# Kernel tuning notes

Measured on AMD Instinct MI355X. Metric: run time of the kernel, lower is better.

The kernel has to match this reference:

```python
import jax, jax.numpy as jnp
import numpy as np

DIM = 1024
NUM_HEADS = 16
HEAD_DIM = DIM // NUM_HEADS


def setup_inputs() -> dict:
    key = jax.random.key(0)
    k1, k2, k3, k4, k5 = jax.random.split(key, 5)
    scale = 0.02
    return {
        "x": jax.random.normal(k1, (4, 2048, DIM), dtype=jnp.float32),
        "w_qkv": jax.random.normal(k2, (DIM, 3 * DIM), dtype=jnp.float32) * scale,
        "b_qkv": jax.random.normal(k3, (3 * DIM,), dtype=jnp.float32) * scale,
        "w_proj": jax.random.normal(k4, (DIM, DIM), dtype=jnp.float32) * scale,
        "b_proj": jax.random.normal(k5, (DIM,), dtype=jnp.float32) * scale,
    }


def reference(x, w_qkv, b_qkv, w_proj, b_proj):
    B, N, C = x.shape
    H, D = NUM_HEADS, HEAD_DIM
    qkv = x @ w_qkv + b_qkv                      # [B, N, 3C]
    qkv = qkv.reshape(B, N, 3, H, D)
    q = qkv[:, :, 0].transpose(0, 2, 1, 3)       # [B, H, N, D]
    k = qkv[:, :, 1].transpose(0, 2, 1, 3)
    v = qkv[:, :, 2].transpose(0, 2, 1, 3)
    attn = jnp.einsum("bhnd,bhmd->bhnm", q, k) / (D ** 0.5)  # [B, H, N, N]
    attn = jax.nn.softmax(attn, axis=-1)
    out = jnp.einsum("bhnm,bhmd->bhnd", attn, v)  # [B, H, N, D]
    out = out.transpose(0, 2, 1, 3).reshape(B, N, C)
    return out @ w_proj + b_proj
```

## Files before the change

### kernel.cpp

```cpp
#include <hip/hip_runtime.h>
#include <stdint.h>

typedef __bf16 bf16_t;
typedef __bf16 bf16x8 __attribute__((ext_vector_type(8)));
typedef __bf16 bf16x4 __attribute__((ext_vector_type(4)));
typedef float  f32x4  __attribute__((ext_vector_type(4)));

__device__ __forceinline__ void g2l16(const void* g, void* l) {
    __builtin_amdgcn_global_load_lds(
        (const __attribute__((address_space(1))) unsigned int*)g,
        (__attribute__((address_space(3))) unsigned int*)l, 16, 0, 0);
}

__global__ __launch_bounds__(256) void prep_kernel(
    const float* __restrict__ x, const float* __restrict__ w_qkv,
    const float* __restrict__ w_proj,
    bf16_t* __restrict__ x_bf, bf16_t* __restrict__ wqkvT, bf16_t* __restrict__ wprojT)
{
    __shared__ float t[32][33];
    const int bx = blockIdx.x;
    if (bx < 8192) {
        const int idx = (bx * 256 + threadIdx.x) * 4;
        const float4 v = *(const float4*)(x + idx);
        bf16x4 o;
        o[0] = (bf16_t)v.x; o[1] = (bf16_t)v.y; o[2] = (bf16_t)v.z; o[3] = (bf16_t)v.w;
        *(bf16x4*)(x_bf + idx) = o;
        return;
    }
    const float* in;
    bf16_t* outp;
    int c0, r0, C;
    if (bx < 11264) {
        const int b = bx - 8192;
        in = w_qkv; outp = wqkvT; C = 3072;
        c0 = (b % 96) * 32; r0 = (b / 96) * 32;
    } else {
        const int b = bx - 11264;
        in = w_proj; outp = wprojT; C = 1024;
        c0 = (b & 31) * 32; r0 = (b >> 5) * 32;
    }
    const int xx = threadIdx.x & 31, y = threadIdx.x >> 5;
    #pragma unroll
    for (int i = 0; i < 32; i += 8)
        t[y + i][xx] = in[(size_t)(r0 + y + i) * C + c0 + xx];
    __syncthreads();
    #pragma unroll
    for (int i = 0; i < 32; i += 8)
        outp[(size_t)(c0 + y + i) * 1024 + r0 + xx] = (bf16_t)t[xx][y + i];
}

__device__ __forceinline__ void gemm128(
    const bf16_t* __restrict__ A, const bf16_t* __restrict__ Bt, const int K,
    bf16_t* sA, bf16_t* sB, const int m0, const int n0, f32x4 acc[4][4])
{
    const int tid  = threadIdx.x;
    const int lane = tid & 63;
    const int w    = tid >> 6;
    const int wm   = (w >> 1) * 64;
    const int wn   = (w & 1) * 64;
    const int col0 = lane & 15;
    const int quad = lane >> 4;

    #pragma unroll
    for (int mt = 0; mt < 4; ++mt)
        #pragma unroll
        for (int nt = 0; nt < 4; ++nt)
            acc[mt][nt] = (f32x4){0.f, 0.f, 0.f, 0.f};

    const int srow = tid >> 3;
    const int jsw  = ((tid & 7) ^ (srow & 7)) << 3;
    const bf16_t* Ab = A  + (size_t)(m0 + srow) * K + jsw;
    const bf16_t* Bb = Bt + (size_t)(n0 + srow) * K + jsw;

    for (int kb = 0; kb < K; kb += 64) {
        #pragma unroll
        for (int it = 0; it < 4; ++it) {
            g2l16(Ab + (size_t)(it * 32) * K + kb, sA + (size_t)(it * 256 + tid) * 8);
            g2l16(Bb + (size_t)(it * 32) * K + kb, sB + (size_t)(it * 256 + tid) * 8);
        }
        __syncthreads();
        #pragma unroll
        for (int ks = 0; ks < 2; ++ks) {
            const int jg = ks * 4 + quad;
            bf16x8 af[4], bv[4];
            #pragma unroll
            for (int mt = 0; mt < 4; ++mt) {
                const int ra = wm + mt * 16 + col0;
                af[mt] = *(const bf16x8*)(sA + ra * 64 + ((jg ^ (ra & 7)) << 3));
            }
            #pragma unroll
            for (int nt = 0; nt < 4; ++nt) {
                const int rb = wn + nt * 16 + col0;
                bv[nt] = *(const bf16x8*)(sB + rb * 64 + ((jg ^ (rb & 7)) << 3));
            }
            #pragma unroll
            for (int mt = 0; mt < 4; ++mt)
                #pragma unroll
                for (int nt = 0; nt < 4; ++nt)
                    acc[mt][nt] = __builtin_amdgcn_mfma_f32_16x16x32_bf16(
                        af[mt], bv[nt], acc[mt][nt], 0, 0, 0);
        }
        __syncthreads();
    }
}

#define QSCALE 0.18033688f
__global__ __launch_bounds__(256) void qkv_gemm_kernel(
    const bf16_t* __restrict__ x, const bf16_t* __restrict__ wT,
    const float* __restrict__ bias,
    bf16_t* __restrict__ q, bf16_t* __restrict__ k, bf16_t* __restrict__ vT)
{
    __shared__ bf16_t sA[128 * 64];
    __shared__ bf16_t sB[128 * 64];
    const int m0 = blockIdx.y * 128;
    const int n0 = blockIdx.x * 128;
    f32x4 acc[4][4];
    gemm128(x, wT, 1024, sA, sB, m0, n0, acc);

    const int tid = threadIdx.x, lane = tid & 63, w = tid >> 6;
    const int wm = (w >> 1) * 64, wn = (w & 1) * 64;
    const int col0 = lane & 15, quad = lane >> 4;
    const int sel = n0 >> 10;

    #pragma unroll
    for (int mt = 0; mt < 4; ++mt) {
        const int m_base = m0 + wm + mt * 16 + quad * 4;
        const int b = m_base >> 11;
        const int t = m_base & 2047;
        #pragma unroll
        for (int nt = 0; nt < 4; ++nt) {
            const int n = n0 + wn + nt * 16 + col0;
            const float bvv = bias[n];
            const int h = (n >> 6) & 15, d = n & 63;
            const size_t bh = (size_t)b * 16 + h;
            if (sel == 0) {
                #pragma unroll
                for (int r = 0; r < 4; ++r)
                    q[(bh * 2048 + t + r) * 64 + d] = (bf16_t)((acc[mt][nt][r] + bvv) * QSCALE);
            } else if (sel == 1) {
                #pragma unroll
                for (int r = 0; r < 4; ++r)
                    k[(bh * 2048 + t + r) * 64 + d] = (bf16_t)(acc[mt][nt][r] + bvv);
            } else {
                #pragma unroll
                for (int r = 0; r < 4; ++r)
                    vT[(bh * 64 + d) * 2048 + t + r] = (bf16_t)(acc[mt][nt][r] + bvv);
            }
        }
    }
}

__global__ __launch_bounds__(256) void proj_gemm_kernel(
    const bf16_t* __restrict__ a, const bf16_t* __restrict__ wT,
    const float* __restrict__ bias, float* __restrict__ out)
{
    __shared__ bf16_t sA[128 * 64];
    __shared__ bf16_t sB[128 * 64];
    const int m0 = blockIdx.y * 128;
    const int n0 = blockIdx.x * 128;
    f32x4 acc[4][4];
    gemm128(a, wT, 1024, sA, sB, m0, n0, acc);

    const int tid = threadIdx.x, lane = tid & 63, w = tid >> 6;
    const int wm = (w >> 1) * 64, wn = (w & 1) * 64;
    const int col0 = lane & 15, quad = lane >> 4;
    #pragma unroll
    for (int mt = 0; mt < 4; ++mt) {
        const int m_base = m0 + wm + mt * 16 + quad * 4;
        #pragma unroll
        for (int nt = 0; nt < 4; ++nt) {
            const int n = n0 + wn + nt * 16 + col0;
            const float bvv = bias[n];
            #pragma unroll
            for (int r = 0; r < 4; ++r)
                out[(size_t)(m_base + r) * 1024 + n] = acc[mt][nt][r] + bvv;
        }
    }
}

#define SP_STRIDE 72
__global__ __launch_bounds__(256, 3) void attn_kernel(
    const bf16_t* __restrict__ q, const bf16_t* __restrict__ k,
    const bf16_t* __restrict__ vT, bf16_t* __restrict__ out)
{
    __shared__ __align__(16) char smem[18432 + 16384 + 16384];
    bf16_t* sQ = (bf16_t*)smem;
    bf16_t* sP = (bf16_t*)smem;
    bf16_t* sK = (bf16_t*)(smem + 18432);
    bf16_t* sV = (bf16_t*)(smem + 18432 + 16384);

    const int x   = blockIdx.x;
    const int loc = x >> 3;
    const int qb  = loc & 15;
    const int bh  = (x & 7) + ((loc >> 4) << 3);

    const int tid = threadIdx.x, lane = tid & 63, w = tid >> 6;
    const int col0 = lane & 15, quad = lane >> 4;

    const bf16_t* qbase = q  + ((size_t)bh * 2048 + qb * 128) * 64;
    const bf16_t* kbase = k  + (size_t)bh * 2048 * 64;
    const bf16_t* vbase = vT + (size_t)bh * 64 * 2048;

    const int srow8  = tid >> 3;
    const int jsw8   = ((tid & 7) ^ (srow8 & 7)) << 3;
    const int srow16 = tid >> 4;
    const int jsw16  = ((tid & 15) ^ (srow16 & 15)) << 3;

    #pragma unroll
    for (int it = 0; it < 4; ++it)
        g2l16(qbase + (size_t)(it * 32 + srow8) * 64 + jsw8,
              sQ + (size_t)(it * 256 + tid) * 8);

    bf16x8 kr[4], vr[4];
    #pragma unroll
    for (int it = 0; it < 4; ++it)
        kr[it] = *(const bf16x8*)(kbase + (size_t)(it * 32 + srow8) * 64 + jsw8);
    #pragma unroll
    for (int it = 0; it < 4; ++it)
        vr[it] = *(const bf16x8*)(vbase + (size_t)(it * 16 + srow16) * 2048 + jsw16);

    __syncthreads();

    bf16x8 qf[2][2];
    #pragma unroll
    for (int mt = 0; mt < 2; ++mt)
        #pragma unroll
        for (int ks = 0; ks < 2; ++ks) {
            const int rq = w * 32 + mt * 16 + col0;
            const int jg = ks * 4 + quad;
            qf[mt][ks] = *(const bf16x8*)(sQ + rq * 64 + ((jg ^ (rq & 7)) << 3));
        }

    f32x4 oacc[2][4];
    float row_l[2][4];
    #pragma unroll
    for (int mt = 0; mt < 2; ++mt) {
        #pragma unroll
        for (int nt = 0; nt < 4; ++nt) oacc[mt][nt] = (f32x4){0.f, 0.f, 0.f, 0.f};
        #pragma unroll
        for (int r = 0; r < 4; ++r) row_l[mt][r] = 0.f;
    }

    for (int kv = 0; kv < 16; ++kv) {
        __syncthreads();
        #pragma unroll
        for (int it = 0; it < 4; ++it)
            *(bf16x8*)(sK + (size_t)(it * 256 + tid) * 8) = kr[it];
        #pragma unroll
        for (int it = 0; it < 4; ++it)
            *(bf16x8*)(sV + (size_t)(it * 256 + tid) * 8) = vr[it];
        __syncthreads();

        const int kvn = (kv < 15) ? kv + 1 : 15;
        const bf16_t* kg = kbase + (size_t)kvn * 128 * 64;
        #pragma unroll
        for (int it = 0; it < 4; ++it)
            kr[it] = *(const bf16x8*)(kg + (size_t)(it * 32 + srow8) * 64 + jsw8);
        #pragma unroll
        for (int it = 0; it < 4; ++it)
            vr[it] = *(const bf16x8*)(vbase + (size_t)(it * 16 + srow16) * 2048
                                      + kvn * 128 + jsw16);

        f32x4 s[2][8];
        #pragma unroll
        for (int mt = 0; mt < 2; ++mt)
            #pragma unroll
            for (int nt = 0; nt < 8; ++nt) s[mt][nt] = (f32x4){0.f, 0.f, 0.f, 0.f};
        #pragma unroll
        for (int ks = 0; ks < 2; ++ks) {
            const int jg = ks * 4 + quad;
            bf16x8 kf[8];
            #pragma unroll
            for (int nt = 0; nt < 8; ++nt) {
                const int rk = nt * 16 + col0;
                kf[nt] = *(const bf16x8*)(sK + rk * 64 + ((jg ^ (rk & 7)) << 3));
            }
            #pragma unroll
            for (int mt = 0; mt < 2; ++mt)
                #pragma unroll
                for (int nt = 0; nt < 8; ++nt)
                    s[mt][nt] = __builtin_amdgcn_mfma_f32_16x16x32_bf16(
                        qf[mt][ks], kf[nt], s[mt][nt], 0, 0, 0);
        }

        #pragma unroll
        for (int mt = 0; mt < 2; ++mt)
            #pragma unroll
            for (int r = 0; r < 4; ++r) {
                float rs = 0.f;
                #pragma unroll
                for (int nt = 0; nt < 8; ++nt) {
                    const float p = __builtin_amdgcn_exp2f(s[mt][nt][r]);
                    s[mt][nt][r] = p;
                    rs += p;
                }
                row_l[mt][r] += rs;
            }

        #pragma unroll
        for (int half = 0; half < 2; ++half) {
            #pragma unroll
            for (int mt = 0; mt < 2; ++mt)
                #pragma unroll
                for (int nt = 0; nt < 4; ++nt)
                    #pragma unroll
                    for (int r = 0; r < 4; ++r)
                        sP[(w * 32 + mt * 16 + quad * 4 + r) * SP_STRIDE + nt * 16 + col0] =
                            (bf16_t)s[mt][half * 4 + nt][r];
            #pragma unroll
            for (int ks = 0; ks < 2; ++ks) {
                bf16x8 pf[2], vf[4];
                #pragma unroll
                for (int mt = 0; mt < 2; ++mt)
                    pf[mt] = *(const bf16x8*)(sP + (w * 32 + mt * 16 + col0) * SP_STRIDE
                                              + ks * 32 + quad * 8);
                #pragma unroll
                for (int nt = 0; nt < 4; ++nt) {
                    const int dv = nt * 16 + col0;
                    const int jg = half * 8 + ks * 4 + quad;
                    vf[nt] = *(const bf16x8*)(sV + dv * 128 + ((jg ^ (dv & 15)) << 3));
                }
                #pragma unroll
                for (int mt = 0; mt < 2; ++mt)
                    #pragma unroll
                    for (int nt = 0; nt < 4; ++nt)
                        oacc[mt][nt] = __builtin_amdgcn_mfma_f32_16x16x32_bf16(
                            pf[mt], vf[nt], oacc[mt][nt], 0, 0, 0);
            }
        }
    }

    const int b = bh >> 4, h = bh & 15;
    #pragma unroll
    for (int mt = 0; mt < 2; ++mt) {
        #pragma unroll
        for (int r = 0; r < 4; ++r) {
            float l = row_l[mt][r];
            #pragma unroll
            for (int off = 1; off < 16; off <<= 1) l += __shfl_xor(l, off);
            const float inv = 1.0f / l;
            const int t = qb * 128 + w * 32 + mt * 16 + quad * 4 + r;
            const size_t rowbase = ((size_t)b * 2048 + t) * 1024 + h * 64;
            #pragma unroll
            for (int nt = 0; nt < 4; ++nt)
                out[rowbase + nt * 16 + col0] = (bf16_t)(oacc[mt][nt][r] * inv);
        }
    }
}

extern "C" void kernel_launch(void* const* d_in, const int* in_sizes, int n_in,
                              void* d_out, int out_size, void* d_ws, size_t ws_size,
                              hipStream_t stream) {
    const float* x      = (const float*)d_in[0];
    const float* w_qkv  = (const float*)d_in[1];
    const float* b_qkv  = (const float*)d_in[2];
    const float* w_proj = (const float*)d_in[3];
    const float* b_proj = (const float*)d_in[4];
    float* out = (float*)d_out;

    char* p = (char*)d_ws;
    bf16_t* x_bf   = (bf16_t*)p; p += (size_t)8192 * 1024 * 2;
    bf16_t* wqkvT  = (bf16_t*)p; p += (size_t)3072 * 1024 * 2;
    bf16_t* wprojT = (bf16_t*)p; p += (size_t)1024 * 1024 * 2;
    bf16_t* qb     = (bf16_t*)p; p += (size_t)8192 * 1024 * 2;
    bf16_t* kb     = (bf16_t*)p; p += (size_t)8192 * 1024 * 2;
    bf16_t* vTb    = (bf16_t*)p; p += (size_t)8192 * 1024 * 2;
    bf16_t* attb   = (bf16_t*)p; p += (size_t)8192 * 1024 * 2;

    prep_kernel<<<12288, 256, 0, stream>>>(x, w_qkv, w_proj, x_bf, wqkvT, wprojT);
    qkv_gemm_kernel<<<dim3(24, 64), 256, 0, stream>>>(x_bf, wqkvT, b_qkv, qb, kb, vTb);
    attn_kernel<<<1024, 256, 0, stream>>>(qb, kb, vTb, attb);
    proj_gemm_kernel<<<dim3(8, 64), 256, 0, stream>>>(attb, wprojT, b_proj, out);
}
```

Measured before the change: 279.7 us.

## Keep softmax probabilities in registers via transposed QK^T and permlane swaps

Computes S transposed (K as the A operand, Q as B) so that each lane holds the scores for a single query row, then converts the probabilities to packed bf16 and rearranges them across lanes with permlane32/16 swaps into the A-operand layout of the PV MFMA. This removes the shared-memory P buffer and its store/load round trip; Q is now loaded straight from global into registers, dropping the Q LDS staging and one barrier. LDS use per block shrinks, which may allow more resident blocks. The lane-shuffle mapping is subtle, and the row-sum reduction now goes through a different shuffle pattern.

```diff
diff --git a/kernel.cpp b/kernel.cpp
--- a/kernel.cpp
+++ b/kernel.cpp
@@ -178,16 +178,13 @@
     }
 }
 
-#define SP_STRIDE 72
 __global__ __launch_bounds__(256, 3) void attn_kernel(
     const bf16_t* __restrict__ q, const bf16_t* __restrict__ k,
     const bf16_t* __restrict__ vT, bf16_t* __restrict__ out)
 {
-    __shared__ __align__(16) char smem[18432 + 16384 + 16384];
-    bf16_t* sQ = (bf16_t*)smem;
-    bf16_t* sP = (bf16_t*)smem;
-    bf16_t* sK = (bf16_t*)(smem + 18432);
-    bf16_t* sV = (bf16_t*)(smem + 18432 + 16384);
+    __shared__ __align__(16) char smem[16384 + 16384];
+    bf16_t* sK = (bf16_t*)smem;
+    bf16_t* sV = (bf16_t*)(smem + 16384);
 
     const int x   = blockIdx.x;
     const int loc = x >> 3;
@@ -206,10 +203,13 @@
     const int srow16 = tid >> 4;
     const int jsw16  = ((tid & 15) ^ (srow16 & 15)) << 3;
 
-    #pragma unroll
-    for (int it = 0; it < 4; ++it)
-        g2l16(qbase + (size_t)(it * 32 + srow8) * 64 + jsw8,
-              sQ + (size_t)(it * 256 + tid) * 8);
+    bf16x8 qf[2][2];
+    #pragma unroll
+    for (int mt = 0; mt < 2; ++mt)
+        #pragma unroll
+        for (int ks = 0; ks < 2; ++ks)
+            qf[mt][ks] = *(const bf16x8*)(qbase
+                + (size_t)(w * 32 + mt * 16 + col0) * 64 + ks * 32 + quad * 8);
 
     bf16x8 kr[4], vr[4];
     #pragma unroll
@@ -219,26 +219,13 @@
     for (int it = 0; it < 4; ++it)
         vr[it] = *(const bf16x8*)(vbase + (size_t)(it * 16 + srow16) * 2048 + jsw16);
 
-    __syncthreads();
-
-    bf16x8 qf[2][2];
-    #pragma unroll
-    for (int mt = 0; mt < 2; ++mt)
-        #pragma unroll
-        for (int ks = 0; ks < 2; ++ks) {
-            const int rq = w * 32 + mt * 16 + col0;
-            const int jg = ks * 4 + quad;
-            qf[mt][ks] = *(const bf16x8*)(sQ + rq * 64 + ((jg ^ (rq & 7)) << 3));
-        }
-
     f32x4 oacc[2][4];
-    float row_l[2][4];
+    float row_l[2];
     #pragma unroll
     for (int mt = 0; mt < 2; ++mt) {
         #pragma unroll
         for (int nt = 0; nt < 4; ++nt) oacc[mt][nt] = (f32x4){0.f, 0.f, 0.f, 0.f};
-        #pragma unroll
-        for (int r = 0; r < 4; ++r) row_l[mt][r] = 0.f;
+        row_l[mt] = 0.f;
     }
 
     for (int kv = 0; kv < 16; ++kv) {
@@ -261,84 +248,95 @@
             vr[it] = *(const bf16x8*)(vbase + (size_t)(it * 16 + srow16) * 2048
                                       + kvn * 128 + jsw16);
 
-        f32x4 s[2][8];
-        #pragma unroll
-        for (int mt = 0; mt < 2; ++mt)
-            #pragma unroll
-            for (int nt = 0; nt < 8; ++nt) s[mt][nt] = (f32x4){0.f, 0.f, 0.f, 0.f};
-        #pragma unroll
-        for (int ks = 0; ks < 2; ++ks) {
-            const int jg = ks * 4 + quad;
-            bf16x8 kf[8];
-            #pragma unroll
-            for (int nt = 0; nt < 8; ++nt) {
-                const int rk = nt * 16 + col0;
-                kf[nt] = *(const bf16x8*)(sK + rk * 64 + ((jg ^ (rk & 7)) << 3));
-            }
-            #pragma unroll
-            for (int mt = 0; mt < 2; ++mt)
-                #pragma unroll
-                for (int nt = 0; nt < 8; ++nt)
-                    s[mt][nt] = __builtin_amdgcn_mfma_f32_16x16x32_bf16(
-                        qf[mt][ks], kf[nt], s[mt][nt], 0, 0, 0);
-        }
-
-        #pragma unroll
-        for (int mt = 0; mt < 2; ++mt)
-            #pragma unroll
-            for (int r = 0; r < 4; ++r) {
-                float rs = 0.f;
-                #pragma unroll
-                for (int nt = 0; nt < 8; ++nt) {
-                    const float p = __builtin_amdgcn_exp2f(s[mt][nt][r]);
-                    s[mt][nt][r] = p;
-                    rs += p;
+        #pragma unroll
+        for (int hf = 0; hf < 2; ++hf) {
+            f32x4 s[4][2];
+            #pragma unroll
+            for (int nt = 0; nt < 4; ++nt)
+                #pragma unroll
+                for (int mt = 0; mt < 2; ++mt) s[nt][mt] = (f32x4){0.f, 0.f, 0.f, 0.f};
+            #pragma unroll
+            for (int ks = 0; ks < 2; ++ks) {
+                const int jg = ks * 4 + quad;
+                bf16x8 kf[4];
+                #pragma unroll
+                for (int nt = 0; nt < 4; ++nt) {
+                    const int rk = hf * 64 + nt * 16 + col0;
+                    kf[nt] = *(const bf16x8*)(sK + rk * 64 + ((jg ^ (rk & 7)) << 3));
                 }
-                row_l[mt][r] += rs;
-            }
-
-        #pragma unroll
-        for (int half = 0; half < 2; ++half) {
-            #pragma unroll
-            for (int mt = 0; mt < 2; ++mt)
                 #pragma unroll
                 for (int nt = 0; nt < 4; ++nt)
                     #pragma unroll
-                    for (int r = 0; r < 4; ++r)
-                        sP[(w * 32 + mt * 16 + quad * 4 + r) * SP_STRIDE + nt * 16 + col0] =
-                            (bf16_t)s[mt][half * 4 + nt][r];
-            #pragma unroll
-            for (int ks = 0; ks < 2; ++ks) {
-                bf16x8 pf[2], vf[4];
-                #pragma unroll
-                for (int mt = 0; mt < 2; ++mt)
-                    pf[mt] = *(const bf16x8*)(sP + (w * 32 + mt * 16 + col0) * SP_STRIDE
-                                              + ks * 32 + quad * 8);
+                    for (int mt = 0; mt < 2; ++mt)
+                        s[nt][mt] = __builtin_amdgcn_mfma_f32_16x16x32_bf16(
+                            kf[nt], qf[mt][ks], s[nt][mt], 0, 0, 0);
+            }
+
+            unsigned pw[2][2][4];
+            #pragma unroll
+            for (int mt = 0; mt < 2; ++mt) {
+                #pragma unroll
+                for (int kp = 0; kp < 2; ++kp) {
+                    float p0[4], p1[4];
+                    float rs = 0.f;
+                    #pragma unroll
+                    for (int r = 0; r < 4; ++r) {
+                        p0[r] = __builtin_amdgcn_exp2f(s[2 * kp][mt][r]);
+                        p1[r] = __builtin_amdgcn_exp2f(s[2 * kp + 1][mt][r]);
+                        rs += p0[r] + p1[r];
+                    }
+                    row_l[mt] += rs;
+                    unsigned XA, XB, YA, YB;
+                    asm("v_cvt_pk_bf16_f32 %0, %1, %2" : "=v"(XA) : "v"(p0[0]), "v"(p0[1]));
+                    asm("v_cvt_pk_bf16_f32 %0, %1, %2" : "=v"(XB) : "v"(p0[2]), "v"(p0[3]));
+                    asm("v_cvt_pk_bf16_f32 %0, %1, %2" : "=v"(YA) : "v"(p1[0]), "v"(p1[1]));
+                    asm("v_cvt_pk_bf16_f32 %0, %1, %2" : "=v"(YB) : "v"(p1[2]), "v"(p1[3]));
+                    asm("v_permlane32_swap_b32 %0, %1" : "+v"(XA), "+v"(YA));
+                    asm("v_permlane16_swap_b32 %0, %1" : "+v"(XA), "+v"(YA));
+                    asm("v_permlane32_swap_b32 %0, %1" : "+v"(XB), "+v"(YB));
+                    asm("v_permlane16_swap_b32 %0, %1" : "+v"(XB), "+v"(YB));
+                    pw[mt][kp][0] = XA; pw[mt][kp][1] = XB;
+                    pw[mt][kp][2] = YA; pw[mt][kp][3] = YB;
+                }
+            }
+
+            #pragma unroll
+            for (int kp = 0; kp < 2; ++kp) {
+                const int jg2 = (hf * 2 + kp) * 4 + quad;
+                bf16x8 vf[4];
                 #pragma unroll
                 for (int nt = 0; nt < 4; ++nt) {
                     const int dv = nt * 16 + col0;
-                    const int jg = half * 8 + ks * 4 + quad;
-                    vf[nt] = *(const bf16x8*)(sV + dv * 128 + ((jg ^ (dv & 15)) << 3));
+                    vf[nt] = *(const bf16x8*)(sV + dv * 128 + ((jg2 ^ (dv & 15)) << 3));
                 }
                 #pragma unroll
-                for (int mt = 0; mt < 2; ++mt)
+                for (int mt = 0; mt < 2; ++mt) {
+                    union { unsigned wds[4]; bf16x8 v; } u;
+                    u.wds[0] = pw[mt][kp][0]; u.wds[1] = pw[mt][kp][1];
+                    u.wds[2] = pw[mt][kp][2]; u.wds[3] = pw[mt][kp][3];
                     #pragma unroll
                     for (int nt = 0; nt < 4; ++nt)
                         oacc[mt][nt] = __builtin_amdgcn_mfma_f32_16x16x32_bf16(
-                            pf[mt], vf[nt], oacc[mt][nt], 0, 0, 0);
-            }
-        }
-    }
-
+                            u.v, vf[nt], oacc[mt][nt], 0, 0, 0);
+                }
+            }
+        }
+    }
+
+    float lt[2];
+    #pragma unroll
+    for (int mt = 0; mt < 2; ++mt) {
+        float l = row_l[mt];
+        l += __shfl_xor(l, 16);
+        l += __shfl_xor(l, 32);
+        lt[mt] = l;
+    }
     const int b = bh >> 4, h = bh & 15;
     #pragma unroll
     for (int mt = 0; mt < 2; ++mt) {
         #pragma unroll
         for (int r = 0; r < 4; ++r) {
-            float l = row_l[mt][r];
-            #pragma unroll
-            for (int off = 1; off < 16; off <<= 1) l += __shfl_xor(l, off);
-            const float inv = 1.0f / l;
+            const float inv = 1.0f / __shfl(lt[mt], quad * 4 + r);
             const int t = qb * 128 + w * 32 + mt * 16 + quad * 4 + r;
             const size_t rowbase = ((size_t)b * 2048 + t) * 1024 + h * 64;
             #pragma unroll
```

New measurement: 291.2 us. +4.1%, slower.
